# Performance work log

Hardware: AMD Instinct MI355X
Metric: run time of the kernel (lower is better)

## Reference

```python
import jax, jax.numpy as jnp
import numpy as np

N = 30000      # nodes
E = 480000     # directed edges (before self loops)
G = 64         # graphs in batch
L = 20         # padded token-list length per node feature
D = 32         # embedding_dim
S = 64         # scalar_feature_count
H, C = 4, 128  # conv1 heads / hidden_channels
TOT = S + 5 * D  # 224
EPS_LN = 1e-5


def setup_inputs() -> dict:
    key = jax.random.key(0)
    ks = jax.random.split(key, 24)
    f32 = jnp.float32
    rn = lambda k, shp: jax.random.normal(k, shp, dtype=f32) * 0.05
    inp = {}
    inp["x_scalar"] = jax.random.normal(ks[0], (N, S), dtype=f32)
    inp["x_opcode"] = jax.random.randint(ks[1], (N, L), 0, 512)
    inp["x_source"] = jax.random.randint(ks[2], (N, L), 0, 256)
    inp["x_sink"] = jax.random.randint(ks[3], (N, L), 0, 256)
    inp["x_string_manip"] = jax.random.randint(ks[4], (N, L), 0, 128)
    inp["x_payload"] = jax.random.randint(ks[5], (N, L), 0, 256)
    inp["edge_index"] = jax.random.randint(ks[6], (2, E), 0, N)
    inp["batch"] = jnp.sort(jax.random.randint(ks[7], (N,), 0, G))
    inp["emb_opcode"] = rn(ks[8], (512, D))
    inp["emb_source"] = rn(ks[9], (256, D))
    inp["emb_sink"] = rn(ks[10], (256, D))
    inp["emb_string"] = rn(ks[11], (128, D))
    inp["emb_payload"] = rn(ks[12], (256, D))
    inp["ln_scale"] = jnp.ones((TOT,), f32)
    inp["ln_bias"] = jnp.zeros((TOT,), f32)
    inp["W1"] = rn(ks[13], (TOT, H * C))
    inp["att_src1"] = rn(ks[14], (H, C))
    inp["att_dst1"] = rn(ks[15], (H, C))
    inp["b1"] = jnp.zeros((H * C,), f32)
    inp["W2"] = rn(ks[16], (H * C, C))
    inp["att_src2"] = rn(ks[17], (1, C))
    inp["att_dst2"] = rn(ks[18], (1, C))
    inp["b2"] = jnp.zeros((C,), f32)
    return inp


def masked_pool(table, idx):
    # padding_idx=0 masked mean over the list dim
    emb = table[idx]                                    # [N, L, D]
    mask = (idx != 0).astype(emb.dtype)[..., None]      # [N, L, 1]
    return (emb * mask).sum(1) / (mask.sum(1) + 1e-9)   # [N, D]


def layer_norm(x, scale, bias):
    mu = x.mean(-1, keepdims=True)
    var = jnp.mean((x - mu) ** 2, -1, keepdims=True)
    return (x - mu) * jax.lax.rsqrt(var + EPS_LN) * scale + bias


def gat_layer(x, src, dst, W, a_src, a_dst, bias, n):
    # PyG GATConv (eval mode, concat=True, negative_slope=0.2)
    heads, c = a_src.shape
    h = (x @ W).reshape(n, heads, c)                    # [N, H, C]
    s = (h * a_src).sum(-1)                             # [N, H]
    d = (h * a_dst).sum(-1)                             # [N, H]
    e = jax.nn.leaky_relu(s[src] + d[dst], 0.2)         # [E, H]
    m = jax.ops.segment_max(e, dst, num_segments=n)     # segment softmax over dst
    ex = jnp.exp(e - m[dst])
    den = jax.ops.segment_sum(ex, dst, num_segments=n)
    alpha = ex / den[dst]                               # [E, H]
    out = jax.ops.segment_sum(alpha[:, :, None] * h[src], dst, num_segments=n)
    return out.reshape(n, heads * c) + bias


def reference(x_scalar, x_opcode, x_source, x_sink, x_string_manip, x_payload,
              edge_index, batch,
              emb_opcode, emb_source, emb_sink, emb_string, emb_payload,
              ln_scale, ln_bias,
              W1, att_src1, att_dst1, b1,
              W2, att_src2, att_dst2, b2):
    n = x_scalar.shape[0]
    feats = jnp.concatenate([
        x_scalar,
        masked_pool(emb_opcode, x_opcode),
        masked_pool(emb_source, x_source),
        masked_pool(emb_sink, x_sink),
        masked_pool(emb_string, x_string_manip),
        masked_pool(emb_payload, x_payload),
    ], axis=1)
    x = layer_norm(feats, ln_scale, ln_bias)
    # PyG GATConv adds self loops by default
    loops = jnp.arange(n)
    src = jnp.concatenate([edge_index[0], loops])
    dst = jnp.concatenate([edge_index[1], loops])
    x = jax.nn.elu(gat_layer(x, src, dst, W1, att_src1, att_dst1, b1, n))
    x = jax.nn.elu(gat_layer(x, src, dst, W2, att_src2, att_dst2, b2, n))
    # global_max_pool over graphs
    return jax.ops.segment_max(x, batch, num_segments=G)
```

## Files before the change

### kernel.cpp

```cpp
#include <hip/hip_runtime.h>
#include <hip/hip_bf16.h>
#include <math.h>

#define N_NODES 30000
#define M_PAD   30016
#define N_EDGES 480000
#define N_GRAPH 64
#define L_TOK   20
#define D_EMB   32
#define S_SCAL  64
#define TOT     224
#define H1      4
#define C1      128
#define F1      512
#define F2      128
#define E_TOT   (N_EDGES + N_NODES)

typedef __attribute__((ext_vector_type(8))) short bf16x8;
typedef __attribute__((ext_vector_type(4))) float f32x4;

__device__ __forceinline__ unsigned short f2b(float f) {
    unsigned u = __float_as_uint(f);
    u += 0x7FFFu + ((u >> 16) & 1u);
    return (unsigned short)(u >> 16);
}
__device__ __forceinline__ float b2f(unsigned short h) {
    return __uint_as_float(((unsigned)h) << 16);
}
__device__ __forceinline__ float blo(unsigned u) { return __uint_as_float(u << 16); }
__device__ __forceinline__ float bhi(unsigned u) { return __uint_as_float(u & 0xFFFF0000u); }

__global__ void init_all(int* deg, float* s1, float* d1, float* s2, float* d2) {
    int i = blockIdx.x * blockDim.x + threadIdx.x;
    if (i < N_NODES) {
        deg[i] = 1;
        s2[i] = 0.f; d2[i] = 0.f;
        float4 z = make_float4(0.f, 0.f, 0.f, 0.f);
        *reinterpret_cast<float4*>(&s1[i * 4]) = z;
        *reinterpret_cast<float4*>(&d1[i * 4]) = z;
    }
}

__global__ void add_deg(const int* __restrict__ ei, int* deg) {
    int e = blockIdx.x * blockDim.x + threadIdx.x;
    if (e < N_EDGES) atomicAdd(&deg[ei[N_EDGES + e]], 1);
}

#define SCAN_PER 30
__global__ void scan_deg(const int* __restrict__ deg, int* __restrict__ rowptr,
                         int* __restrict__ cursor) {
    int t = threadIdx.x, lane = t & 63, wid = t >> 6;
    int base = t * SCAN_PER;
    int v[SCAN_PER];
    int lsum = 0;
    #pragma unroll
    for (int i = 0; i < SCAN_PER; ++i) {
        int ii = base + i;
        int d = (ii < N_NODES) ? deg[ii] : 0;
        v[i] = lsum;
        lsum += d;
    }
    int incl = lsum;
    #pragma unroll
    for (int off = 1; off < 64; off <<= 1) {
        int u = __shfl_up(incl, off);
        if (lane >= off) incl += u;
    }
    __shared__ int wsum[16], woff[16];
    if (lane == 63) wsum[wid] = incl;
    __syncthreads();
    if (t == 0) {
        int run = 0;
        #pragma unroll
        for (int w = 0; w < 16; ++w) { woff[w] = run; run += wsum[w]; }
        rowptr[N_NODES] = run;
    }
    __syncthreads();
    int texcl = woff[wid] + (incl - lsum);
    #pragma unroll
    for (int i = 0; i < SCAN_PER; ++i) {
        int ii = base + i;
        if (ii < N_NODES) { int p = texcl + v[i]; rowptr[ii] = p; cursor[ii] = p; }
    }
}

__global__ void scatter_edges(const int* __restrict__ ei, int* cursor, int* csr_src) {
    int e = blockIdx.x * blockDim.x + threadIdx.x;
    if (e < N_EDGES) {
        int src = ei[e], dst = ei[N_EDGES + e];
        int pos = atomicAdd(&cursor[dst], 1);
        csr_src[pos] = src;
    } else if (e < E_TOT) {
        int n = e - N_EDGES;
        int pos = atomicAdd(&cursor[n], 1);
        csr_src[pos] = n;
    }
}

__global__ void transpose_cast(const float* __restrict__ W, unsigned short* __restrict__ WT,
                               int K, int N) {
    __shared__ float tile[32][33];
    int kb = blockIdx.x * 32, nb = blockIdx.y * 32;
    int t = threadIdx.x;
    int r = t >> 3, c4 = (t & 7) * 4;
    float4 v = *reinterpret_cast<const float4*>(&W[(size_t)(kb + r) * N + nb + c4]);
    tile[r][c4 + 0] = v.x; tile[r][c4 + 1] = v.y;
    tile[r][c4 + 2] = v.z; tile[r][c4 + 3] = v.w;
    __syncthreads();
    ushort4 o;
    o.x = f2b(tile[c4 + 0][r]); o.y = f2b(tile[c4 + 1][r]);
    o.z = f2b(tile[c4 + 2][r]); o.w = f2b(tile[c4 + 3][r]);
    *reinterpret_cast<ushort4*>(&WT[(size_t)(nb + r) * K + kb + c4]) = o;
}

__global__ void feat_ln(const float* __restrict__ xs,
                        const int* __restrict__ xo, const int* __restrict__ xsrc,
                        const int* __restrict__ xsink, const int* __restrict__ xstr,
                        const int* __restrict__ xpay,
                        const float* __restrict__ eo, const float* __restrict__ es,
                        const float* __restrict__ ek, const float* __restrict__ eg,
                        const float* __restrict__ ep,
                        const float* __restrict__ lns, const float* __restrict__ lnb,
                        unsigned short* __restrict__ x0) {
    int node = blockIdx.x * 4 + (threadIdx.x >> 6);
    if (node >= N_NODES) return;
    int lane = threadIdx.x & 63;
    int c = lane * 4;
    float f0 = 0.f, f1 = 0.f, f2 = 0.f, f3 = 0.f;
    if (lane < 16) {
        float4 v = *reinterpret_cast<const float4*>(&xs[(size_t)node * S_SCAL + c]);
        f0 = v.x; f1 = v.y; f2 = v.z; f3 = v.w;
    } else if (lane < 56) {
        int t = c - S_SCAL;
        int ti = t >> 5, dim = t & 31;
        const int* idx; const float* emb;
        switch (ti) {
            case 0: idx = xo;   emb = eo; break;
            case 1: idx = xsrc; emb = es; break;
            case 2: idx = xsink;emb = ek; break;
            case 3: idx = xstr; emb = eg; break;
            default:idx = xpay; emb = ep; break;
        }
        float a0 = 0.f, a1 = 0.f, a2 = 0.f, a3 = 0.f, cnt = 0.f;
        #pragma unroll
        for (int l = 0; l < L_TOK; ++l) {
            int id = idx[node * L_TOK + l];
            if (id != 0) {
                float4 e = *reinterpret_cast<const float4*>(&emb[id * D_EMB + dim]);
                a0 += e.x; a1 += e.y; a2 += e.z; a3 += e.w; cnt += 1.f;
            }
        }
        float r = 1.f / (cnt + 1e-9f);
        f0 = a0 * r; f1 = a1 * r; f2 = a2 * r; f3 = a3 * r;
    }
    float s = f0 + f1 + f2 + f3;
    float q = f0 * f0 + f1 * f1 + f2 * f2 + f3 * f3;
    #pragma unroll
    for (int off = 32; off; off >>= 1) {
        s += __shfl_xor(s, off);
        q += __shfl_xor(q, off);
    }
    float mu = s * (1.f / (float)TOT);
    float var = q * (1.f / (float)TOT) - mu * mu;
    float rs = rsqrtf(var + 1e-5f);
    if (lane < 56) {
        float4 sc = *reinterpret_cast<const float4*>(&lns[c]);
        float4 bi = *reinterpret_cast<const float4*>(&lnb[c]);
        ushort4 o;
        o.x = f2b((f0 - mu) * rs * sc.x + bi.x);
        o.y = f2b((f1 - mu) * rs * sc.y + bi.y);
        o.z = f2b((f2 - mu) * rs * sc.z + bi.z);
        o.w = f2b((f3 - mu) * rs * sc.w + bi.w);
        *reinterpret_cast<ushort4*>(&x0[(size_t)node * TOT + c]) = o;
    }
}

__global__ void gemm_bf16(const unsigned short* __restrict__ A,
                          const unsigned short* __restrict__ BT,
                          unsigned short* __restrict__ C, int M, int N, int K,
                          const float* __restrict__ asrc, const float* __restrict__ adst,
                          float* __restrict__ sOut, float* __restrict__ dOut, int H) {
    __shared__ unsigned short As[64][40];
    __shared__ unsigned short Bs[64][40];
    int tid = threadIdx.x;
    int wave = tid >> 6, lane = tid & 63;
    int l15 = lane & 15, kb = lane >> 4;
    int bm = blockIdx.x * 64, bn = blockIdx.y * 64;
    f32x4 acc[4] = {};
    int row_ld = tid >> 2, seg = tid & 3;
    for (int k0 = 0; k0 < K; k0 += 32) {
        {
            const uint4 v = *reinterpret_cast<const uint4*>(&A[(size_t)(bm + row_ld) * K + k0 + seg * 8]);
            *reinterpret_cast<uint4*>(&As[row_ld][seg * 8]) = v;
        }
        {
            const uint4 v = *reinterpret_cast<const uint4*>(&BT[(size_t)(bn + row_ld) * K + k0 + seg * 8]);
            *reinterpret_cast<uint4*>(&Bs[row_ld][seg * 8]) = v;
        }
        __syncthreads();
        bf16x8 af = *reinterpret_cast<const bf16x8*>(&As[wave * 16 + l15][kb * 8]);
        #pragma unroll
        for (int t = 0; t < 4; ++t) {
            bf16x8 bfr = *reinterpret_cast<const bf16x8*>(&Bs[t * 16 + l15][kb * 8]);
            acc[t] = __builtin_amdgcn_mfma_f32_16x16x32_bf16(af, bfr, acc[t], 0, 0, 0);
        }
        __syncthreads();
    }
    #pragma unroll
    for (int t = 0; t < 4; ++t) {
        #pragma unroll
        for (int r = 0; r < 4; ++r) {
            int row = bm + wave * 16 + kb * 4 + r;
            if (row < M)
                C[(size_t)row * N + bn + t * 16 + l15] = f2b(acc[t][r]);
        }
    }
    {
        float a_s[4], a_d[4];
        #pragma unroll
        for (int t = 0; t < 4; ++t) {
            a_s[t] = asrc[bn + t * 16 + l15];
            a_d[t] = adst[bn + t * 16 + l15];
        }
        int head = bn / (N / H);
        #pragma unroll
        for (int r = 0; r < 4; ++r) {
            float ps = acc[0][r] * a_s[0] + acc[1][r] * a_s[1]
                     + acc[2][r] * a_s[2] + acc[3][r] * a_s[3];
            float pd = acc[0][r] * a_d[0] + acc[1][r] * a_d[1]
                     + acc[2][r] * a_d[2] + acc[3][r] * a_d[3];
            #pragma unroll
            for (int off = 8; off >= 1; off >>= 1) {
                ps += __shfl_xor(ps, off);
                pd += __shfl_xor(pd, off);
            }
            if (l15 == 0) {
                int row = bm + wave * 16 + kb * 4 + r;
                if (row < M) {
                    atomicAdd(&sOut[row * H + head], ps);
                    atomicAdd(&dOut[row * H + head], pd);
                }
            }
        }
    }
}

#define ACC8(v, a) \
    acc[0] += (a) * blo((v).x); acc[1] += (a) * bhi((v).x); \
    acc[2] += (a) * blo((v).y); acc[3] += (a) * bhi((v).y); \
    acc[4] += (a) * blo((v).z); acc[5] += (a) * bhi((v).z); \
    acc[6] += (a) * blo((v).w); acc[7] += (a) * bhi((v).w);

__global__ void gat1_aggregate(const unsigned short* __restrict__ h1, const float* __restrict__ s1,
                               const float* __restrict__ d1, const int* __restrict__ rowptr,
                               const int* __restrict__ csr, const float* __restrict__ b1,
                               unsigned short* __restrict__ x1) {
    int n = blockIdx.x, tid = threadIdx.x;
    int wave = tid >> 6, lane = tid & 63;
    int head = lane >> 4;
    int r0 = rowptr[n], deg = rowptr[n + 1] - r0;
    __shared__ float alpha_sh[H1][68];
    __shared__ int src_sh[64];
    __shared__ float d_n[H1];
    __shared__ float red[3][512];
    if (tid < H1) d_n[tid] = d1[n * H1 + tid];
    __syncthreads();
    float dnw = d_n[wave];
    const uint4* h1u4 = (const uint4*)h1;
    float acc[8] = {};

    auto gather = [&](int cnt) {
        int iA = wave, iB = wave + 4, iC = wave + 8, iD = wave + 12;
        bool hA = iA < cnt, hB = iB < cnt, hC = iC < cnt, hD = iD < cnt;
        int s; float aA, aB, aC, aD; uint4 vA, vB, vC, vD;
        if (hA) { s = __builtin_amdgcn_readfirstlane(src_sh[iA]); aA = alpha_sh[head][iA]; vA = h1u4[(size_t)s * 64 + lane]; }
        if (hB) { s = __builtin_amdgcn_readfirstlane(src_sh[iB]); aB = alpha_sh[head][iB]; vB = h1u4[(size_t)s * 64 + lane]; }
        if (hC) { s = __builtin_amdgcn_readfirstlane(src_sh[iC]); aC = alpha_sh[head][iC]; vC = h1u4[(size_t)s * 64 + lane]; }
        if (hD) { s = __builtin_amdgcn_readfirstlane(src_sh[iD]); aD = alpha_sh[head][iD]; vD = h1u4[(size_t)s * 64 + lane]; }
        while (hA) {
            {
                uint4 v = vA; float a = aA;
                iA += 16; hA = iA < cnt;
                if (hA) { s = __builtin_amdgcn_readfirstlane(src_sh[iA]); aA = alpha_sh[head][iA]; vA = h1u4[(size_t)s * 64 + lane]; }
                ACC8(v, a)
            }
            if (hB) {
                uint4 v = vB; float a = aB;
                iB += 16; hB = iB < cnt;
                if (hB) { s = __builtin_amdgcn_readfirstlane(src_sh[iB]); aB = alpha_sh[head][iB]; vB = h1u4[(size_t)s * 64 + lane]; }
                ACC8(v, a)
            }
            if (hC) {
                uint4 v = vC; float a = aC;
                iC += 16; hC = iC < cnt;
                if (hC) { s = __builtin_amdgcn_readfirstlane(src_sh[iC]); aC = alpha_sh[head][iC]; vC = h1u4[(size_t)s * 64 + lane]; }
                ACC8(v, a)
            }
            if (hD) {
                uint4 v = vD; float a = aD;
                iD += 16; hD = iD < cnt;
                if (hD) { s = __builtin_amdgcn_readfirstlane(src_sh[iD]); aD = alpha_sh[head][iD]; vD = h1u4[(size_t)s * 64 + lane]; }
                ACC8(v, a)
            }
        }
    };

    if (deg <= 64) {
        float e = -1e30f;
        if (lane < deg) {
            int src = csr[r0 + lane];
            if (wave == 0) src_sh[lane] = src;
            float ev = s1[src * H1 + wave] + dnw;
            e = (ev >= 0.f) ? ev : 0.2f * ev;
        }
        float m = e;
        #pragma unroll
        for (int off = 32; off; off >>= 1) m = fmaxf(m, __shfl_xor(m, off));
        float ex = (lane < deg) ? __expf(e - m) : 0.f;
        float den = ex;
        #pragma unroll
        for (int off = 32; off; off >>= 1) den += __shfl_xor(den, off);
        alpha_sh[wave][lane] = ex / den;
        __syncthreads();
        gather(deg);
    } else {
        float m = -1e30f;
        for (int i = lane; i < deg; i += 64) {
            int src = csr[r0 + i];
            float e = s1[src * H1 + wave] + dnw;
            e = (e >= 0.f) ? e : 0.2f * e;
            m = fmaxf(m, e);
        }
        #pragma unroll
        for (int off = 32; off; off >>= 1) m = fmaxf(m, __shfl_xor(m, off));
        float den = 0.f;
        for (int i = lane; i < deg; i += 64) {
            int src = csr[r0 + i];
            float e = s1[src * H1 + wave] + dnw;
            e = (e >= 0.f) ? e : 0.2f * e;
            den += __expf(e - m);
        }
        #pragma unroll
        for (int off = 32; off; off >>= 1) den += __shfl_xor(den, off);
        float invw = 1.f / den;
        for (int c0 = 0; c0 < deg; c0 += 64) {
            __syncthreads();
            int i = c0 + lane;
            if (i < deg) {
                int src = csr[r0 + i];
                if (wave == 0) src_sh[lane] = src;
                float e = s1[src * H1 + wave] + dnw;
                e = (e >= 0.f) ? e : 0.2f * e;
                alpha_sh[wave][lane] = __expf(e - m) * invw;
            }
            __syncthreads();
            gather(min(64, deg - c0));
        }
    }
    if (wave > 0) {
        *reinterpret_cast<float4*>(&red[wave - 1][lane * 4]) =
            make_float4(acc[0], acc[1], acc[2], acc[3]);
        *reinterpret_cast<float4*>(&red[wave - 1][256 + lane * 4]) =
            make_float4(acc[4], acc[5], acc[6], acc[7]);
    }
    __syncthreads();
    if (wave == 0) {
        #pragma unroll
        for (int w = 0; w < 3; ++w) {
            float4 p = *reinterpret_cast<float4*>(&red[w][lane * 4]);
            float4 q = *reinterpret_cast<float4*>(&red[w][256 + lane * 4]);
            acc[0] += p.x; acc[1] += p.y; acc[2] += p.z; acc[3] += p.w;
            acc[4] += q.x; acc[5] += q.y; acc[6] += q.z; acc[7] += q.w;
        }
        float4 b0 = *reinterpret_cast<const float4*>(&b1[lane * 8]);
        float4 b4 = *reinterpret_cast<const float4*>(&b1[lane * 8 + 4]);
        float v0 = acc[0] + b0.x; v0 = (v0 > 0.f) ? v0 : expm1f(v0);
        float v1 = acc[1] + b0.y; v1 = (v1 > 0.f) ? v1 : expm1f(v1);
        float v2 = acc[2] + b0.z; v2 = (v2 > 0.f) ? v2 : expm1f(v2);
        float v3 = acc[3] + b0.w; v3 = (v3 > 0.f) ? v3 : expm1f(v3);
        float v4 = acc[4] + b4.x; v4 = (v4 > 0.f) ? v4 : expm1f(v4);
        float v5 = acc[5] + b4.y; v5 = (v5 > 0.f) ? v5 : expm1f(v5);
        float v6 = acc[6] + b4.z; v6 = (v6 > 0.f) ? v6 : expm1f(v6);
        float v7 = acc[7] + b4.w; v7 = (v7 > 0.f) ? v7 : expm1f(v7);
        uint4 pk;
        pk.x = (unsigned)f2b(v0) | ((unsigned)f2b(v1) << 16);
        pk.y = (unsigned)f2b(v2) | ((unsigned)f2b(v3) << 16);
        pk.z = (unsigned)f2b(v4) | ((unsigned)f2b(v5) << 16);
        pk.w = (unsigned)f2b(v6) | ((unsigned)f2b(v7) << 16);
        ((uint4*)x1)[(size_t)n * 64 + lane] = pk;
    }
}

__global__ void gat2_node(const unsigned short* __restrict__ h2, const float* __restrict__ s2,
                          const float* __restrict__ d2, const int* __restrict__ rowptr,
                          const int* __restrict__ csr, const float* __restrict__ b2,
                          float* __restrict__ h2act) {
    int n = blockIdx.x, tid = threadIdx.x;
    int wid = tid >> 6, lane = tid & 63;
    int grp = tid >> 4, l16 = tid & 15;
    int r0 = rowptr[n], deg = rowptr[n + 1] - r0;
    __shared__ float alpha_sh[128];
    __shared__ int src_sh[128];
    __shared__ float rA[2], rB[2];
    __shared__ float red[8][128];
    float dn = d2[n];
    const uint4* h2u4 = (const uint4*)h2;
    float acc[8] = {};

    auto gather = [&](int cnt) {
        int iA = grp, iB = grp + 8;
        bool hA = iA < cnt, hB = iB < cnt;
        int sA, sB; float aA, aB; uint4 vA, vB;
        if (hA) { sA = src_sh[iA]; aA = alpha_sh[iA]; vA = h2u4[(size_t)sA * 16 + l16]; }
        if (hB) { sB = src_sh[iB]; aB = alpha_sh[iB]; vB = h2u4[(size_t)sB * 16 + l16]; }
        while (hA) {
            {
                uint4 v = vA; float a = aA;
                iA += 16; hA = iA < cnt;
                if (hA) { sA = src_sh[iA]; aA = alpha_sh[iA]; vA = h2u4[(size_t)sA * 16 + l16]; }
                ACC8(v, a)
            }
            if (hB) {
                uint4 v = vB; float a = aB;
                iB += 16; hB = iB < cnt;
                if (hB) { sB = src_sh[iB]; aB = alpha_sh[iB]; vB = h2u4[(size_t)sB * 16 + l16]; }
                ACC8(v, a)
            }
        }
    };

    if (deg <= 128) {
        float e = -1e30f;
        if (tid < deg) {
            int src = csr[r0 + tid];
            src_sh[tid] = src;
            float ev = s2[src] + dn;
            e = (ev >= 0.f) ? ev : 0.2f * ev;
        }
        float m = e;
        #pragma unroll
        for (int off = 32; off; off >>= 1) m = fmaxf(m, __shfl_xor(m, off));
        if (lane == 0) rA[wid] = m;
        __syncthreads();
        m = fmaxf(rA[0], rA[1]);
        float ex = (tid < deg) ? __expf(e - m) : 0.f;
        float den = ex;
        #pragma unroll
        for (int off = 32; off; off >>= 1) den += __shfl_xor(den, off);
        if (lane == 0) rB[wid] = den;
        __syncthreads();
        den = rB[0] + rB[1];
        alpha_sh[tid] = ex / den;
        __syncthreads();
        gather(deg);
    } else {
        float m = -1e30f;
        for (int i = tid; i < deg; i += 128) {
            float e = s2[csr[r0 + i]] + dn; e = (e >= 0.f) ? e : 0.2f * e;
            m = fmaxf(m, e);
        }
        #pragma unroll
        for (int off = 32; off; off >>= 1) m = fmaxf(m, __shfl_xor(m, off));
        if (lane == 0) rA[wid] = m;
        __syncthreads();
        m = fmaxf(rA[0], rA[1]);
        float den = 0.f;
        for (int i = tid; i < deg; i += 128) {
            float e = s2[csr[r0 + i]] + dn; e = (e >= 0.f) ? e : 0.2f * e;
            den += __expf(e - m);
        }
        #pragma unroll
        for (int off = 32; off; off >>= 1) den += __shfl_xor(den, off);
        if (lane == 0) rB[wid] = den;
        __syncthreads();
        den = rB[0] + rB[1];
        float inv = 1.f / den;
        for (int c0 = 0; c0 < deg; c0 += 128) {
            __syncthreads();
            int i = c0 + tid;
            if (i < deg) {
                int src = csr[r0 + i];
                src_sh[tid] = src;
                float e = s2[src] + dn; e = (e >= 0.f) ? e : 0.2f * e;
                alpha_sh[tid] = __expf(e - m) * inv;
            }
            __syncthreads();
            gather(min(128, deg - c0));
        }
    }
    *reinterpret_cast<float4*>(&red[grp][l16 * 4]) =
        make_float4(acc[0], acc[1], acc[2], acc[3]);
    *reinterpret_cast<float4*>(&red[grp][64 + l16 * 4]) =
        make_float4(acc[4], acc[5], acc[6], acc[7]);
    __syncthreads();
    {
        int pos = tid;
        int ch = (pos < 64) ? ((pos >> 2) * 8 + (pos & 3))
                            : (((pos - 64) >> 2) * 8 + 4 + (pos & 3));
        float s = red[0][pos] + red[1][pos] + red[2][pos] + red[3][pos]
                + red[4][pos] + red[5][pos] + red[6][pos] + red[7][pos] + b2[ch];
        s = (s > 0.f) ? s : expm1f(s);
        h2act[(size_t)n * F2 + ch] = s;
    }
}

__global__ void graph_pool(const float* __restrict__ h2act, const int* __restrict__ batch,
                           float* __restrict__ out) {
    int gph = blockIdx.x;
    int tid = threadIdx.x;
    __shared__ int se[2];
    __shared__ float red[128];
    if (tid < 2) {
        int target = gph + tid;
        int lo = 0, hi = N_NODES;
        while (lo < hi) { int mid = (lo + hi) >> 1; if (batch[mid] < target) lo = mid + 1; else hi = mid; }
        se[tid] = lo;
    }
    __syncthreads();
    int start = se[0], end = se[1];
    int ch = tid & 127, noff = tid >> 7;
    float m = -INFINITY;
    for (int i = start + noff; i < end; i += 2)
        m = fmaxf(m, h2act[(size_t)i * F2 + ch]);
    if (noff == 1) red[ch] = m;
    __syncthreads();
    if (noff == 0) out[gph * F2 + ch] = fmaxf(m, red[ch]);
}

extern "C" void kernel_launch(void* const* d_in, const int* in_sizes, int n_in,
                              void* d_out, int out_size, void* d_ws, size_t ws_size,
                              hipStream_t stream) {
    const float* x_scalar = (const float*)d_in[0];
    const int*   x_opcode = (const int*)d_in[1];
    const int*   x_source = (const int*)d_in[2];
    const int*   x_sink   = (const int*)d_in[3];
    const int*   x_string = (const int*)d_in[4];
    const int*   x_payload= (const int*)d_in[5];
    const int*   edge_idx = (const int*)d_in[6];
    const int*   batch    = (const int*)d_in[7];
    const float* emb_op   = (const float*)d_in[8];
    const float* emb_src  = (const float*)d_in[9];
    const float* emb_snk  = (const float*)d_in[10];
    const float* emb_str  = (const float*)d_in[11];
    const float* emb_pay  = (const float*)d_in[12];
    const float* ln_scale = (const float*)d_in[13];
    const float* ln_bias  = (const float*)d_in[14];
    const float* W1       = (const float*)d_in[15];
    const float* att_src1 = (const float*)d_in[16];
    const float* att_dst1 = (const float*)d_in[17];
    const float* b1       = (const float*)d_in[18];
    const float* W2       = (const float*)d_in[19];
    const float* att_src2 = (const float*)d_in[20];
    const float* att_dst2 = (const float*)d_in[21];
    const float* b2       = (const float*)d_in[22];
    float* out = (float*)d_out;

    unsigned short* x0  = (unsigned short*)d_ws;
    unsigned short* h1  = x0 + (size_t)M_PAD * TOT;
    unsigned short* x1  = h1 + (size_t)M_PAD * F1;
    unsigned short* h2  = x1 + (size_t)M_PAD * F1;
    unsigned short* W1T = h2 + (size_t)M_PAD * F2;
    unsigned short* W2T = W1T + (size_t)F1 * TOT;
    float* s1 = (float*)(W2T + (size_t)F2 * F1);
    float* d1 = s1 + (size_t)N_NODES * H1;
    float* s2 = d1 + (size_t)N_NODES * H1;
    float* d2 = s2 + N_NODES;
    int* rowptr = (int*)(d2 + N_NODES);
    int* cursor = rowptr + (N_NODES + 1);
    int* csr    = cursor + (N_NODES + 1);
    float* h2act = (float*)x1;

    init_all<<<(N_NODES + 255) / 256, 256, 0, stream>>>(cursor, s1, d1, s2, d2);
    add_deg<<<(N_EDGES + 255) / 256, 256, 0, stream>>>(edge_idx, cursor);
    scan_deg<<<1, 1024, 0, stream>>>(cursor, rowptr, cursor);
    scatter_edges<<<(E_TOT + 255) / 256, 256, 0, stream>>>(edge_idx, cursor, csr);

    dim3 t1(TOT / 32, F1 / 32);
    transpose_cast<<<t1, 256, 0, stream>>>(W1, W1T, TOT, F1);
    dim3 t2(F1 / 32, F2 / 32);
    transpose_cast<<<t2, 256, 0, stream>>>(W2, W2T, F1, F2);

    feat_ln<<<(N_NODES + 3) / 4, 256, 0, stream>>>(x_scalar, x_opcode, x_source, x_sink,
                                                   x_string, x_payload, emb_op, emb_src,
                                                   emb_snk, emb_str, emb_pay, ln_scale,
                                                   ln_bias, x0);

    dim3 g1(M_PAD / 64, F1 / 64);
    gemm_bf16<<<g1, 256, 0, stream>>>(x0, W1T, h1, N_NODES, F1, TOT,
                                      att_src1, att_dst1, s1, d1, H1);
    gat1_aggregate<<<N_NODES, 256, 0, stream>>>(h1, s1, d1, rowptr, csr, b1, x1);

    dim3 g2(M_PAD / 64, F2 / 64);
    gemm_bf16<<<g2, 256, 0, stream>>>(x1, W2T, h2, N_NODES, F2, F1,
                                      att_src2, att_dst2, s2, d2, 1);

    gat2_node<<<N_NODES, 128, 0, stream>>>(h2, s2, d2, rowptr, csr, b2, h2act);
    graph_pool<<<N_GRAPH, 256, 0, stream>>>(h2act, batch, out);
}
```

Measured before the change: 343.4 us.

## Enlarge GEMM tiles with direct-to-LDS loads, merge transposes, deepen gat2 gather

The bf16 GEMM moves from 64x64 to 128x128 tiles, with each wave computing a 4x4 grid of MFMA tiles. Operands are loaded straight into LDS through global_load_lds using an XOR swizzle, and M_PAD grows to a multiple of 128. The two weight-transpose launches become one kernel, and the gat2 gather keeps four loads in flight per lane instead of two. The aim is more operand reuse, fewer launches and better latency hiding, at the cost of more registers and fewer GEMM blocks to spread over the GPU (gemm2 has only 235 of them).

```diff
diff --git a/kernel.cpp b/kernel.cpp
--- a/kernel.cpp
+++ b/kernel.cpp
@@ -3,7 +3,7 @@
 #include <math.h>
 
 #define N_NODES 30000
-#define M_PAD   30016
+#define M_PAD   30080
 #define N_EDGES 480000
 #define N_GRAPH 64
 #define L_TOK   20
@@ -29,6 +29,12 @@
 }
 __device__ __forceinline__ float blo(unsigned u) { return __uint_as_float(u << 16); }
 __device__ __forceinline__ float bhi(unsigned u) { return __uint_as_float(u & 0xFFFF0000u); }
+
+__device__ __forceinline__ void gload_lds16(const void* g, void* l) {
+    __builtin_amdgcn_global_load_lds(
+        (const __attribute__((address_space(1))) unsigned int*)g,
+        (__attribute__((address_space(3))) unsigned int*)l, 16, 0, 0);
+}
 
 __global__ void init_all(int* deg, float* s1, float* d1, float* s2, float* d2) {
     int i = blockIdx.x * blockDim.x + threadIdx.x;
@@ -97,10 +103,19 @@
     }
 }
 
-__global__ void transpose_cast(const float* __restrict__ W, unsigned short* __restrict__ WT,
-                               int K, int N) {
+__global__ void transpose_cast2(const float* __restrict__ Wa, unsigned short* __restrict__ WaT,
+                                const float* __restrict__ Wb, unsigned short* __restrict__ WbT) {
     __shared__ float tile[32][33];
-    int kb = blockIdx.x * 32, nb = blockIdx.y * 32;
+    int bid = blockIdx.x;
+    const float* W; unsigned short* WT; int K, N, kb, nb;
+    if (bid < (TOT / 32) * (F1 / 32)) {
+        W = Wa; WT = WaT; K = TOT; N = F1;
+        kb = (bid % (TOT / 32)) * 32; nb = (bid / (TOT / 32)) * 32;
+    } else {
+        bid -= (TOT / 32) * (F1 / 32);
+        W = Wb; WT = WbT; K = F1; N = F2;
+        kb = (bid % (F1 / 32)) * 32; nb = (bid / (F1 / 32)) * 32;
+    }
     int t = threadIdx.x;
     int r = t >> 3, c4 = (t & 7) * 4;
     float4 v = *reinterpret_cast<const float4*>(&W[(size_t)(kb + r) * N + nb + c4]);
@@ -180,65 +195,83 @@
                           unsigned short* __restrict__ C, int M, int N, int K,
                           const float* __restrict__ asrc, const float* __restrict__ adst,
                           float* __restrict__ sOut, float* __restrict__ dOut, int H) {
-    __shared__ unsigned short As[64][40];
-    __shared__ unsigned short Bs[64][40];
+    __shared__ unsigned short As[128 * 32];
+    __shared__ unsigned short Bs[128 * 32];
     int tid = threadIdx.x;
-    int wave = tid >> 6, lane = tid & 63;
+    int w = tid >> 6, lane = tid & 63;
     int l15 = lane & 15, kb = lane >> 4;
-    int bm = blockIdx.x * 64, bn = blockIdx.y * 64;
-    f32x4 acc[4] = {};
-    int row_ld = tid >> 2, seg = tid & 3;
+    int wr = w >> 1, wc = w & 1;
+    int bm = blockIdx.x * 128, bn = blockIdx.y * 128;
+    f32x4 acc[4][4] = {};
+    int lrow = lane >> 2, lslot = lane & 3;
+
     for (int k0 = 0; k0 < K; k0 += 32) {
-        {
-            const uint4 v = *reinterpret_cast<const uint4*>(&A[(size_t)(bm + row_ld) * K + k0 + seg * 8]);
-            *reinterpret_cast<uint4*>(&As[row_ld][seg * 8]) = v;
-        }
-        {
-            const uint4 v = *reinterpret_cast<const uint4*>(&BT[(size_t)(bn + row_ld) * K + k0 + seg * 8]);
-            *reinterpret_cast<uint4*>(&Bs[row_ld][seg * 8]) = v;
-        }
-        __syncthreads();
-        bf16x8 af = *reinterpret_cast<const bf16x8*>(&As[wave * 16 + l15][kb * 8]);
-        #pragma unroll
-        for (int t = 0; t < 4; ++t) {
-            bf16x8 bfr = *reinterpret_cast<const bf16x8*>(&Bs[t * 16 + l15][kb * 8]);
-            acc[t] = __builtin_amdgcn_mfma_f32_16x16x32_bf16(af, bfr, acc[t], 0, 0, 0);
-        }
+        #pragma unroll
+        for (int j = 0; j < 2; ++j) {
+            int rbase = w * 16 + j * 64;
+            int row = rbase + lrow;
+            int scol = (lslot ^ (row & 3)) * 8;
+            gload_lds16(&A[(size_t)(bm + row) * K + k0 + scol], &As[rbase * 32]);
+            gload_lds16(&BT[(size_t)(bn + row) * K + k0 + scol], &Bs[rbase * 32]);
+        }
+        __syncthreads();
+        bf16x8 af[4], bf[4];
+        #pragma unroll
+        for (int m = 0; m < 4; ++m) {
+            int row = wr * 64 + m * 16 + l15;
+            af[m] = *reinterpret_cast<const bf16x8*>(&As[row * 32 + (kb ^ (row & 3)) * 8]);
+        }
+        #pragma unroll
+        for (int n = 0; n < 4; ++n) {
+            int row = wc * 64 + n * 16 + l15;
+            bf[n] = *reinterpret_cast<const bf16x8*>(&Bs[row * 32 + (kb ^ (row & 3)) * 8]);
+        }
+        #pragma unroll
+        for (int m = 0; m < 4; ++m)
+            #pragma unroll
+            for (int n = 0; n < 4; ++n)
+                acc[m][n] = __builtin_amdgcn_mfma_f32_16x16x32_bf16(af[m], bf[n], acc[m][n], 0, 0, 0);
         __syncthreads();
     }
     #pragma unroll
-    for (int t = 0; t < 4; ++t) {
+    for (int m = 0; m < 4; ++m) {
         #pragma unroll
         for (int r = 0; r < 4; ++r) {
-            int row = bm + wave * 16 + kb * 4 + r;
-            if (row < M)
-                C[(size_t)row * N + bn + t * 16 + l15] = f2b(acc[t][r]);
+            int row = bm + wr * 64 + m * 16 + kb * 4 + r;
+            if (row < M) {
+                #pragma unroll
+                for (int n = 0; n < 4; ++n)
+                    C[(size_t)row * N + bn + wc * 64 + n * 16 + l15] = f2b(acc[m][n][r]);
+            }
         }
     }
     {
         float a_s[4], a_d[4];
         #pragma unroll
-        for (int t = 0; t < 4; ++t) {
-            a_s[t] = asrc[bn + t * 16 + l15];
-            a_d[t] = adst[bn + t * 16 + l15];
+        for (int n = 0; n < 4; ++n) {
+            a_s[n] = asrc[bn + wc * 64 + n * 16 + l15];
+            a_d[n] = adst[bn + wc * 64 + n * 16 + l15];
         }
         int head = bn / (N / H);
         #pragma unroll
-        for (int r = 0; r < 4; ++r) {
-            float ps = acc[0][r] * a_s[0] + acc[1][r] * a_s[1]
-                     + acc[2][r] * a_s[2] + acc[3][r] * a_s[3];
-            float pd = acc[0][r] * a_d[0] + acc[1][r] * a_d[1]
-                     + acc[2][r] * a_d[2] + acc[3][r] * a_d[3];
+        for (int m = 0; m < 4; ++m) {
             #pragma unroll
-            for (int off = 8; off >= 1; off >>= 1) {
-                ps += __shfl_xor(ps, off);
-                pd += __shfl_xor(pd, off);
-            }
-            if (l15 == 0) {
-                int row = bm + wave * 16 + kb * 4 + r;
-                if (row < M) {
-                    atomicAdd(&sOut[row * H + head], ps);
-                    atomicAdd(&dOut[row * H + head], pd);
+            for (int r = 0; r < 4; ++r) {
+                float ps = acc[m][0][r] * a_s[0] + acc[m][1][r] * a_s[1]
+                         + acc[m][2][r] * a_s[2] + acc[m][3][r] * a_s[3];
+                float pd = acc[m][0][r] * a_d[0] + acc[m][1][r] * a_d[1]
+                         + acc[m][2][r] * a_d[2] + acc[m][3][r] * a_d[3];
+                #pragma unroll
+                for (int off = 8; off >= 1; off >>= 1) {
+                    ps += __shfl_xor(ps, off);
+                    pd += __shfl_xor(pd, off);
+                }
+                if (l15 == 0) {
+                    int row = bm + wr * 64 + m * 16 + kb * 4 + r;
+                    if (row < M) {
+                        atomicAdd(&sOut[row * H + head], ps);
+                        atomicAdd(&dOut[row * H + head], pd);
+                    }
                 }
             }
         }
@@ -408,22 +441,36 @@
     float acc[8] = {};
 
     auto gather = [&](int cnt) {
-        int iA = grp, iB = grp + 8;
-        bool hA = iA < cnt, hB = iB < cnt;
-        int sA, sB; float aA, aB; uint4 vA, vB;
-        if (hA) { sA = src_sh[iA]; aA = alpha_sh[iA]; vA = h2u4[(size_t)sA * 16 + l16]; }
-        if (hB) { sB = src_sh[iB]; aB = alpha_sh[iB]; vB = h2u4[(size_t)sB * 16 + l16]; }
+        int iA = grp, iB = grp + 8, iC = grp + 16, iD = grp + 24;
+        bool hA = iA < cnt, hB = iB < cnt, hC = iC < cnt, hD = iD < cnt;
+        int s; float aA, aB, aC, aD; uint4 vA, vB, vC, vD;
+        if (hA) { s = src_sh[iA]; aA = alpha_sh[iA]; vA = h2u4[(size_t)s * 16 + l16]; }
+        if (hB) { s = src_sh[iB]; aB = alpha_sh[iB]; vB = h2u4[(size_t)s * 16 + l16]; }
+        if (hC) { s = src_sh[iC]; aC = alpha_sh[iC]; vC = h2u4[(size_t)s * 16 + l16]; }
+        if (hD) { s = src_sh[iD]; aD = alpha_sh[iD]; vD = h2u4[(size_t)s * 16 + l16]; }
         while (hA) {
             {
                 uint4 v = vA; float a = aA;
-                iA += 16; hA = iA < cnt;
-                if (hA) { sA = src_sh[iA]; aA = alpha_sh[iA]; vA = h2u4[(size_t)sA * 16 + l16]; }
+                iA += 32; hA = iA < cnt;
+                if (hA) { s = src_sh[iA]; aA = alpha_sh[iA]; vA = h2u4[(size_t)s * 16 + l16]; }
                 ACC8(v, a)
             }
             if (hB) {
                 uint4 v = vB; float a = aB;
-                iB += 16; hB = iB < cnt;
-                if (hB) { sB = src_sh[iB]; aB = alpha_sh[iB]; vB = h2u4[(size_t)sB * 16 + l16]; }
+                iB += 32; hB = iB < cnt;
+                if (hB) { s = src_sh[iB]; aB = alpha_sh[iB]; vB = h2u4[(size_t)s * 16 + l16]; }
+                ACC8(v, a)
+            }
+            if (hC) {
+                uint4 v = vC; float a = aC;
+                iC += 32; hC = iC < cnt;
+                if (hC) { s = src_sh[iC]; aC = alpha_sh[iC]; vC = h2u4[(size_t)s * 16 + l16]; }
+                ACC8(v, a)
+            }
+            if (hD) {
+                uint4 v = vD; float a = aD;
+                iD += 32; hD = iD < cnt;
+                if (hD) { s = src_sh[iD]; aD = alpha_sh[iD]; vD = h2u4[(size_t)s * 16 + l16]; }
                 ACC8(v, a)
             }
         }
@@ -575,22 +622,20 @@
     scan_deg<<<1, 1024, 0, stream>>>(cursor, rowptr, cursor);
     scatter_edges<<<(E_TOT + 255) / 256, 256, 0, stream>>>(edge_idx, cursor, csr);
 
-    dim3 t1(TOT / 32, F1 / 32);
-    transpose_cast<<<t1, 256, 0, stream>>>(W1, W1T, TOT, F1);
-    dim3 t2(F1 / 32, F2 / 32);
-    transpose_cast<<<t2, 256, 0, stream>>>(W2, W2T, F1, F2);
+    transpose_cast2<<<(TOT / 32) * (F1 / 32) + (F1 / 32) * (F2 / 32), 256, 0, stream>>>(
+        W1, W1T, W2, W2T);
 
     feat_ln<<<(N_NODES + 3) / 4, 256, 0, stream>>>(x_scalar, x_opcode, x_source, x_sink,
                                                    x_string, x_payload, emb_op, emb_src,
                                                    emb_snk, emb_str, emb_pay, ln_scale,
                                                    ln_bias, x0);
 
-    dim3 g1(M_PAD / 64, F1 / 64);
+    dim3 g1(M_PAD / 128, F1 / 128);
     gemm_bf16<<<g1, 256, 0, stream>>>(x0, W1T, h1, N_NODES, F1, TOT,
                                       att_src1, att_dst1, s1, d1, H1);
     gat1_aggregate<<<N_NODES, 256, 0, stream>>>(h1, s1, d1, rowptr, csr, b1, x1);
 
-    dim3 g2(M_PAD / 64, F2 / 64);
+    dim3 g2(M_PAD / 128, F2 / 128);
     gemm_bf16<<<g2, 256, 0, stream>>>(x1, W2T, h2, N_NODES, F2, F1,
                                       att_src2, att_dst2, s2, d2, 1);
 
```

New measurement: 342.8 us. About the same (-0.2%).
